# Kernel optimization log

Measured on AMD Instinct MI355X. Metric: run time of the kernel, lower is better.

The kernel has to match this reference:

```python
import jax, jax.numpy as jnp
import numpy as np

B, S, D_IN, D_OUT, ENC, K = 4, 2048, 4096, 4096, 256, 2048


def setup_inputs() -> dict:
    key = jax.random.key(0)
    ks = jax.random.split(key, 10)
    return {
        "x": jax.random.normal(ks[0], (B, S, D_IN), jnp.float32),
        "W": jax.random.normal(ks[1], (D_OUT, D_IN), jnp.float32) * 0.02,
        "b": jax.random.normal(ks[2], (D_OUT,), jnp.float32) * 0.02,
        "enc_W1": jax.random.normal(ks[3], (ENC, D_IN), jnp.float32) * 0.02,
        "enc_b1": jax.random.normal(ks[4], (ENC,), jnp.float32) * 0.02,
        "enc_W2": jax.random.normal(ks[5], (ENC, ENC), jnp.float32) * 0.05,
        "enc_b2": jax.random.normal(ks[6], (ENC,), jnp.float32) * 0.02,
        "keys": jax.random.normal(ks[7], (K, ENC), jnp.float32),
        "values": jax.random.normal(ks[8], (K, D_OUT), jnp.float32),
        "epsilons": jax.random.uniform(ks[9], (K,), jnp.float32) * 20.0,
    }


def reference(x, W, b, enc_W1, enc_b1, enc_W2, enc_b2, keys, values, epsilons):
    # 1) wrapped Linear layer: layer_out = x @ W^T + b   [B,S,D_OUT]
    layer_out = jnp.einsum("bsd,od->bso", x, W) + b

    Bv, Sv = x.shape[0], x.shape[1]
    token_to_edit = Sv - 1  # key_id == -1 inference path

    # 2) per-sample first-diff-position detection (vectorized version of the
    #    python loop: first j>=1 with hs[i,j-1] != hs[i,j], 1 remapped to 0,
    #    and 0 when batch size is 1)
    if Bv == 1:
        first = jnp.zeros((Bv,), jnp.int32)
    else:
        diffs = jnp.any(x[:, 1:] != x[:, :-1], axis=-1)  # [B, S-1]
        has = jnp.any(diffs, axis=1)
        first = jnp.where(has, jnp.argmax(diffs, axis=1).astype(jnp.int32) + 1, 0)
        first = jnp.where(first == 1, 0, first)

    # 3) mean over positions [first_diff_pos, token_to_edit] per sample
    pos = jnp.arange(Sv)
    mask = (pos[None, :] >= first[:, None]) & (pos[None, :] <= token_to_edit)
    m = mask[..., None].astype(x.dtype)
    pooled = (x * m).sum(axis=1) / m.sum(axis=1)  # [B, D_IN]

    # 4) encoder MLP: Linear -> ReLU -> Linear  (MLPEncoder(key_shape, 256))
    h = jax.nn.relu(pooled @ enc_W1.T + enc_b1)
    query = h @ enc_W2.T + enc_b2  # [B, ENC]

    # 5) cdist(keys, query, p=2) -> [K, B], nearest key per sample
    d2 = ((keys * keys).sum(1)[:, None]
          + (query * query).sum(1)[None, :]
          - 2.0 * keys @ query.T)
    dists = jnp.sqrt(jnp.maximum(d2, 0.0))  # [K, B]
    smallest_dist = dists.min(axis=0)        # [B]
    chosen_key = dists.argmin(axis=0)        # [B]

    chosen_value = values[chosen_key]        # [B, D_OUT]
    eps = epsilons[chosen_key]               # [B]

    # 6) replacement == 'replace_all'
    hit = (smallest_dist <= eps)[:, None, None]
    out = jnp.where(hit, chosen_value[:, None, :], layer_out)
    return out
```

## Files before the change

### kernel.cpp

```cpp
#include <hip/hip_runtime.h>
#include <cfloat>
#include <climits>


typedef unsigned short u16;
typedef unsigned int   u32;
typedef __attribute__((ext_vector_type(8))) short bf16x8;
typedef __attribute__((ext_vector_type(4))) float f32x4;
typedef __attribute__((address_space(3))) u32 as3u32;
typedef const __attribute__((address_space(1))) u32 as1u32;

#define NB 4
#define NS 2048
#define ND 4096
#define NE 256
#define NK 2048
#define NROWS (NB * NS)

#define OFF_XB     ((size_t)0)
#define OFF_WB     ((size_t)67108864)
#define OFF_FLAGS  ((size_t)100663296)
#define OFF_FIRST  ((size_t)100696064)
#define OFF_INV    ((size_t)100696080)
#define OFF_POOLED ((size_t)100696320)
#define OFF_H      ((size_t)100761856)
#define OFF_Q      ((size_t)100765952)
#define OFF_CD2    ((size_t)100770048)
#define OFF_CIDX   ((size_t)100770560)
#define OFF_HIT    ((size_t)100771072)
#define OFF_CHOSEN ((size_t)100771088)

__device__ __forceinline__ void gld_lds16(const u16* g, u16* l) {
  __builtin_amdgcn_global_load_lds((as1u32*)g, (as3u32*)l, 16, 0, 0);
}

__device__ __forceinline__ u16 f2bf(float f) {
  union { float f; u32 u; } v; v.f = f;
  u32 r = v.u + 0x7fffu + ((v.u >> 16) & 1u);
  return (u16)(r >> 16);
}

__device__ __forceinline__ void mfma_bf16(f32x4& acc, bf16x8 a, bf16x8 b) {
  asm("v_mfma_f32_16x16x32_bf16 %0, %1, %2, %0" : "+v"(acc) : "v"(a), "v"(b));
}

__global__ __launch_bounds__(256) void k_convert(
    const float* __restrict__ x, const float* __restrict__ W,
    u16* __restrict__ xb, u16* __restrict__ wb, int* __restrict__ flags)
{
  int r = blockIdx.x;
  int tid = threadIdx.x;
  bool isX = r < NROWS;
  int s = r & (NS - 1);
  const float* src;
  u16* dst;
  if (isX) { src = x + (size_t)r * ND; dst = xb + (size_t)r * ND; }
  else     { int wr = r - NROWS; src = W + (size_t)wr * ND; dst = wb + (size_t)wr * ND; }

  const float4* s4 = (const float4*)src;
  int b4 = tid * 4;
  float4 v[4];
#pragma unroll
  for (int i = 0; i < 4; i++) v[i] = s4[b4 + i];

  bool d = false;
  if (isX && s > 0) {
    const float4* p4 = s4 - (ND / 4);
#pragma unroll
    for (int i = 0; i < 4; i++) {
      float4 p = p4[b4 + i];
      d = d || (v[i].x != p.x) || (v[i].y != p.y) || (v[i].z != p.z) || (v[i].w != p.w);
    }
  }

  u16 t[16];
#pragma unroll
  for (int i = 0; i < 4; i++) {
    t[i*4+0] = f2bf(v[i].x); t[i*4+1] = f2bf(v[i].y);
    t[i*4+2] = f2bf(v[i].z); t[i*4+3] = f2bf(v[i].w);
  }
  uint4* d4 = (uint4*)(dst + (size_t)tid * 16);
  d4[0] = *(const uint4*)&t[0];
  d4[1] = *(const uint4*)&t[8];

  if (isX) {
    __shared__ int sf;
    if (tid == 0) sf = 0;
    __syncthreads();
    if (__any((int)d) && (tid & 63) == 0) atomicOr(&sf, 1);
    __syncthreads();
    if (tid == 0) flags[r] = (s == 0) ? 0 : sf;
  }
}

__global__ __launch_bounds__(256) void k_first(
    const int* __restrict__ flags, int* __restrict__ first, float* __restrict__ inv)
{
  __shared__ int red[256];
  int tid = threadIdx.x;
  for (int b = 0; b < NB; b++) {
    int best = INT_MAX;
    for (int j = 1 + tid; j < NS; j += 256)
      if (flags[b * NS + j] && j < best) best = j;
    red[tid] = best;
    __syncthreads();
    for (int st = 128; st > 0; st >>= 1) {
      if (tid < st && red[tid + st] < red[tid]) red[tid] = red[tid + st];
      __syncthreads();
    }
    if (tid == 0) {
      int f = red[0];
      if (f == INT_MAX) f = 0;
      if (f == 1) f = 0;
      first[b] = f;
      inv[b] = 1.0f / (float)(NS - f);
    }
    __syncthreads();
  }
}

__global__ __launch_bounds__(256) void k_pool(
    const float* __restrict__ x, const int* __restrict__ first, float* __restrict__ pooled)
{
  int b = blockIdx.x >> 6;
  int tile = blockIdx.x & 63;
  int f = first[b];
  int s0 = tile * 32;
  int tid = threadIdx.x;
  float acc[16];
#pragma unroll
  for (int k = 0; k < 16; k++) acc[k] = 0.f;
  const float* base = x + ((size_t)b * NS + s0) * ND + tid * 16;
  for (int i = 0; i < 32; i++) {
    if (s0 + i >= f) {
      const float4* p = (const float4*)(base + (size_t)i * ND);
#pragma unroll
      for (int j = 0; j < 4; j++) {
        float4 v = p[j];
        acc[j*4+0] += v.x; acc[j*4+1] += v.y; acc[j*4+2] += v.z; acc[j*4+3] += v.w;
      }
    }
  }
  float* dst = pooled + b * ND + tid * 16;
#pragma unroll
  for (int k = 0; k < 16; k++) atomicAdd(&dst[k], acc[k]);
}

__global__ __launch_bounds__(256) void k_enc1(
    const float* __restrict__ pooled, const float* __restrict__ inv,
    const float* __restrict__ W1, const float* __restrict__ b1, float* __restrict__ h)
{
  int o = blockIdx.x, tid = threadIdx.x;
  const float4* w4 = (const float4*)(W1 + (size_t)o * ND);
  float4 w[4];
#pragma unroll
  for (int i = 0; i < 4; i++) w[i] = w4[tid * 4 + i];
  float part[NB];
#pragma unroll
  for (int b = 0; b < NB; b++) {
    const float4* p4 = (const float4*)(pooled + b * ND);
    float s = 0.f;
#pragma unroll
    for (int i = 0; i < 4; i++) {
      float4 p = p4[tid * 4 + i];
      s += w[i].x*p.x + w[i].y*p.y + w[i].z*p.z + w[i].w*p.w;
    }
    part[b] = s;
  }
  __shared__ float red[NB][4];
  int lane = tid & 63, wv = tid >> 6;
#pragma unroll
  for (int b = 0; b < NB; b++) {
    float v = part[b];
    for (int off = 32; off > 0; off >>= 1) v += __shfl_down(v, off);
    if (lane == 0) red[b][wv] = v;
  }
  __syncthreads();
  if (tid < NB) {
    float s = red[tid][0] + red[tid][1] + red[tid][2] + red[tid][3];
    h[tid * NE + o] = fmaxf(s * inv[tid] + b1[o], 0.f);
  }
}

__global__ __launch_bounds__(256) void k_enc2(
    const float* __restrict__ h, const float* __restrict__ W2,
    const float* __restrict__ b2, float* __restrict__ q)
{
  __shared__ float hs[NB * NE];
  int tid = threadIdx.x;
  for (int i = tid; i < NB * NE; i += 256) hs[i] = h[i];
  __syncthreads();
  const float* w = W2 + (size_t)tid * NE;
  float bb = b2[tid];
  float s0 = bb, s1 = bb, s2 = bb, s3 = bb;
  for (int e = 0; e < NE; e++) {
    float wv = w[e];
    s0 += hs[e] * wv; s1 += hs[NE + e] * wv;
    s2 += hs[2*NE + e] * wv; s3 += hs[3*NE + e] * wv;
  }
  q[tid] = s0; q[NE + tid] = s1; q[2*NE + tid] = s2; q[3*NE + tid] = s3;
}

__global__ __launch_bounds__(64) void k_dist(
    const float* __restrict__ keys, const float* __restrict__ q,
    float* __restrict__ cd2, int* __restrict__ cidx)
{
  __shared__ float qs[NB * NE];
  int tid = threadIdx.x;
  for (int i = tid; i < NB * NE; i += 64) qs[i] = q[i];
  __syncthreads();
  int k = blockIdx.x * 64 + tid;
  const float4* kr = (const float4*)(keys + (size_t)k * NE);
  float d2[NB];
#pragma unroll
  for (int b = 0; b < NB; b++) d2[b] = 0.f;
  for (int e4 = 0; e4 < NE / 4; e4++) {
    float4 kv = kr[e4];
#pragma unroll
    for (int b = 0; b < NB; b++) {
      const float4* qv4 = (const float4*)(qs + b * NE);
      float4 qv = qv4[e4];
      float dx = kv.x - qv.x, dy = kv.y - qv.y, dz = kv.z - qv.z, dw = kv.w - qv.w;
      d2[b] += dx*dx + dy*dy + dz*dz + dw*dw;
    }
  }
#pragma unroll
  for (int b = 0; b < NB; b++) {
    float v = d2[b]; int idx = k;
    for (int off = 32; off > 0; off >>= 1) {
      float ov = __shfl_down(v, off);
      int   oi = __shfl_down(idx, off);
      if (ov < v || (ov == v && oi < idx)) { v = ov; idx = oi; }
    }
    if (tid == 0) { cd2[blockIdx.x * NB + b] = v; cidx[blockIdx.x * NB + b] = idx; }
  }
}

__global__ __launch_bounds__(64) void k_decide(
    const float* __restrict__ cd2, const int* __restrict__ cidx,
    const float* __restrict__ eps, int* __restrict__ hit, int* __restrict__ chosen)
{
  int tid = threadIdx.x;
  for (int b = 0; b < NB; b++) {
    float v = FLT_MAX; int idx = INT_MAX;
    if (tid < 32) { v = cd2[tid * NB + b]; idx = cidx[tid * NB + b]; }
    for (int off = 32; off > 0; off >>= 1) {
      float ov = __shfl_down(v, off);
      int   oi = __shfl_down(idx, off);
      if (ov < v || (ov == v && oi < idx)) { v = ov; idx = oi; }
    }
    if (tid == 0) {
      float dist = sqrtf(fmaxf(v, 0.f));
      chosen[b] = idx;
      hit[b] = (dist <= eps[idx]) ? 1 : 0;
    }
  }
}

__global__ __launch_bounds__(256) void k_gemm(
    const u16* __restrict__ A, const u16* __restrict__ Bw,
    const float* __restrict__ bias, const float* __restrict__ values,
    const int* __restrict__ hit, const int* __restrict__ chosen,
    float* __restrict__ out)
{
  __shared__ __align__(16) u16 As[128 * 64];
  __shared__ __align__(16) u16 Bs[128 * 64];
  int tid = threadIdx.x;
  size_t mbase = (size_t)blockIdx.y * 128;
  size_t nbase = (size_t)blockIdx.x * 128;
  int lane = tid & 63, wv = tid >> 6;
  int wm = (wv >> 1) * 64, wn = (wv & 1) * 64;
  int frow = lane & 15, fk = (lane >> 4) * 8;

  f32x4 acc[4][4] = {};

  for (int kt = 0; kt < ND; kt += 64) {
#pragma unroll
    for (int i = 0; i < 4; i++) {
      int c = i * 256 + tid;
      int row = c >> 3, col = (c & 7) * 8;
      gld_lds16(A  + (mbase + row) * ND + kt + col, &As[c * 8]);
      gld_lds16(Bw + (nbase + row) * ND + kt + col, &Bs[c * 8]);
    }
    __syncthreads();
#pragma unroll
    for (int ks = 0; ks < 2; ks++) {
      bf16x8 af[4], bg[4];
      int ko = ks * 32 + fk;
#pragma unroll
      for (int mf = 0; mf < 4; mf++)
        af[mf] = *(const bf16x8*)&As[(wm + mf * 16 + frow) * 64 + ko];
#pragma unroll
      for (int nf = 0; nf < 4; nf++)
        bg[nf] = *(const bf16x8*)&Bs[(wn + nf * 16 + frow) * 64 + ko];
#pragma unroll
      for (int mf = 0; mf < 4; mf++)
#pragma unroll
        for (int nf = 0; nf < 4; nf++)
          mfma_bf16(acc[mf][nf], af[mf], bg[nf]);
    }
    __syncthreads();
  }

  int smp = (int)(mbase >> 11);
  int ht = hit[smp];
  const float* vrow = values + (size_t)chosen[smp] * ND;
  int r0 = (lane >> 4) * 4, c0 = lane & 15;
#pragma unroll
  for (int mf = 0; mf < 4; mf++) {
    size_t m = mbase + wm + mf * 16 + r0;
#pragma unroll
    for (int nf = 0; nf < 4; nf++) {
      size_t o = nbase + wn + nf * 16 + c0;
      float bia = bias[o];
      float rep = ht ? vrow[o] : 0.f;
#pragma unroll
      for (int r = 0; r < 4; r++) {
        float vvv = acc[mf][nf][r] + bia;
        out[(m + r) * ND + o] = ht ? rep : vvv;
      }
    }
  }
}

extern "C" void kernel_launch(void* const* d_in, const int* in_sizes, int n_in,
                              void* d_out, int out_size, void* d_ws, size_t ws_size,
                              hipStream_t stream) {
  const float* x      = (const float*)d_in[0];
  const float* W      = (const float*)d_in[1];
  const float* bias   = (const float*)d_in[2];
  const float* W1     = (const float*)d_in[3];
  const float* b1     = (const float*)d_in[4];
  const float* W2     = (const float*)d_in[5];
  const float* b2     = (const float*)d_in[6];
  const float* keys   = (const float*)d_in[7];
  const float* values = (const float*)d_in[8];
  const float* eps    = (const float*)d_in[9];
  float* out = (float*)d_out;
  char* ws = (char*)d_ws;

  u16*   xb     = (u16*)(ws + OFF_XB);
  u16*   wb     = (u16*)(ws + OFF_WB);
  int*   flags  = (int*)(ws + OFF_FLAGS);
  int*   first  = (int*)(ws + OFF_FIRST);
  float* inv    = (float*)(ws + OFF_INV);
  float* pooled = (float*)(ws + OFF_POOLED);
  float* h      = (float*)(ws + OFF_H);
  float* q      = (float*)(ws + OFF_Q);
  float* cd2    = (float*)(ws + OFF_CD2);
  int*   cidx   = (int*)(ws + OFF_CIDX);
  int*   hitp   = (int*)(ws + OFF_HIT);
  int*   chosenp= (int*)(ws + OFF_CHOSEN);

  hipMemsetAsync(pooled, 0, NB * ND * sizeof(float), stream);

  k_convert<<<NROWS + ND, 256, 0, stream>>>(x, W, xb, wb, flags);
  k_first  <<<1, 256, 0, stream>>>(flags, first, inv);
  k_pool   <<<256, 256, 0, stream>>>(x, first, pooled);
  k_enc1   <<<NE, 256, 0, stream>>>(pooled, inv, W1, b1, h);
  k_enc2   <<<1, 256, 0, stream>>>(h, W2, b2, q);
  k_dist   <<<NK / 64, 64, 0, stream>>>(keys, q, cd2, cidx);
  k_decide <<<1, 64, 0, stream>>>(cd2, cidx, eps, hitp, chosenp);

  dim3 gg(ND / 128, NROWS / 128);
  k_gemm<<<gg, 256, 0, stream>>>(xb, wb, bias, values, hitp, chosenp, out);
}
```

Before: 741.9 us.

## Rewrite pipeline: fuse pooling into prep, 256x256 ping-pong GEMM, atomic argmin

```diff
diff --git a/kernel.cpp b/kernel.cpp
--- a/kernel.cpp
+++ b/kernel.cpp
@@ -5,6 +5,7 @@
 
 typedef unsigned short u16;
 typedef unsigned int   u32;
+typedef unsigned long long u64;
 typedef __attribute__((ext_vector_type(8))) short bf16x8;
 typedef __attribute__((ext_vector_type(4))) float f32x4;
 typedef __attribute__((address_space(3))) u32 as3u32;
@@ -16,19 +17,17 @@
 #define NE 256
 #define NK 2048
 #define NROWS (NB * NS)
+#define NT 64
 
 #define OFF_XB     ((size_t)0)
 #define OFF_WB     ((size_t)67108864)
-#define OFF_FLAGS  ((size_t)100663296)
-#define OFF_FIRST  ((size_t)100696064)
-#define OFF_INV    ((size_t)100696080)
-#define OFF_POOLED ((size_t)100696320)
-#define OFF_H      ((size_t)100761856)
-#define OFF_Q      ((size_t)100765952)
-#define OFF_CD2    ((size_t)100770048)
-#define OFF_CIDX   ((size_t)100770560)
-#define OFF_HIT    ((size_t)100771072)
-#define OFF_CHOSEN ((size_t)100771088)
+#define OFF_TS     ((size_t)100663296)
+#define OFF_FLAGS  ((size_t)104857600)
+#define OFF_FIRST  ((size_t)104890368)
+#define OFF_INV    ((size_t)104890384)
+#define OFF_MINPK  ((size_t)104890400)
+#define OFF_POOLED ((size_t)104890432)
+#define OFF_H      ((size_t)104955968)
 
 __device__ __forceinline__ void gld_lds16(const u16* g, u16* l) {
   __builtin_amdgcn_global_load_lds((as1u32*)g, (as3u32*)l, 16, 0, 0);
@@ -44,60 +43,86 @@
   asm("v_mfma_f32_16x16x32_bf16 %0, %1, %2, %0" : "+v"(acc) : "v"(a), "v"(b));
 }
 
-__global__ __launch_bounds__(256) void k_convert(
+__global__ __launch_bounds__(256) void k_prep(
     const float* __restrict__ x, const float* __restrict__ W,
-    u16* __restrict__ xb, u16* __restrict__ wb, int* __restrict__ flags)
-{
-  int r = blockIdx.x;
-  int tid = threadIdx.x;
-  bool isX = r < NROWS;
-  int s = r & (NS - 1);
-  const float* src;
-  u16* dst;
-  if (isX) { src = x + (size_t)r * ND; dst = xb + (size_t)r * ND; }
-  else     { int wr = r - NROWS; src = W + (size_t)wr * ND; dst = wb + (size_t)wr * ND; }
-
-  const float4* s4 = (const float4*)src;
-  int b4 = tid * 4;
-  float4 v[4];
-#pragma unroll
-  for (int i = 0; i < 4; i++) v[i] = s4[b4 + i];
-
-  bool d = false;
-  if (isX && s > 0) {
-    const float4* p4 = s4 - (ND / 4);
-#pragma unroll
-    for (int i = 0; i < 4; i++) {
-      float4 p = p4[b4 + i];
-      d = d || (v[i].x != p.x) || (v[i].y != p.y) || (v[i].z != p.z) || (v[i].w != p.w);
-    }
-  }
-
-  u16 t[16];
-#pragma unroll
-  for (int i = 0; i < 4; i++) {
-    t[i*4+0] = f2bf(v[i].x); t[i*4+1] = f2bf(v[i].y);
-    t[i*4+2] = f2bf(v[i].z); t[i*4+3] = f2bf(v[i].w);
-  }
-  uint4* d4 = (uint4*)(dst + (size_t)tid * 16);
-  d4[0] = *(const uint4*)&t[0];
-  d4[1] = *(const uint4*)&t[8];
-
-  if (isX) {
-    __shared__ int sf;
-    if (tid == 0) sf = 0;
-    __syncthreads();
-    if (__any((int)d) && (tid & 63) == 0) atomicOr(&sf, 1);
-    __syncthreads();
-    if (tid == 0) flags[r] = (s == 0) ? 0 : sf;
-  }
+    u16* __restrict__ xb, u16* __restrict__ wb,
+    int* __restrict__ flags, float* __restrict__ ts)
+{
+  int blk = blockIdx.x, tid = threadIdx.x;
+  if (blk >= 256) {
+    int wr0 = (blk - 256) * 16;
+    for (int i = 0; i < 16; i++) {
+      const float* rp = W + (size_t)(wr0 + i) * ND;
+      u16* op = wb + (size_t)(wr0 + i) * ND;
+#pragma unroll
+      for (int ch = 0; ch < 4; ch++) {
+        int col = ch * 1024 + tid * 4;
+        float4 v = *(const float4*)(rp + col);
+        uint2 pk;
+        pk.x = (u32)f2bf(v.x) | ((u32)f2bf(v.y) << 16);
+        pk.y = (u32)f2bf(v.z) | ((u32)f2bf(v.w) << 16);
+        *(uint2*)(op + col) = pk;
+      }
+    }
+    return;
+  }
+  int b = blk >> 6, tile = blk & 63, s0 = tile * 32;
+  __shared__ int rflag[32];
+  if (tid < 32) rflag[tid] = 0;
+  __syncthreads();
+  float prev[16];
+  bool havePrev = (s0 > 0);
+  if (havePrev) {
+    const float* pr = x + ((size_t)b * NS + s0 - 1) * ND;
+#pragma unroll
+    for (int ch = 0; ch < 4; ch++)
+      *(float4*)&prev[ch * 4] = *(const float4*)(pr + ch * 1024 + tid * 4);
+  }
+  float tsa[16];
+#pragma unroll
+  for (int k = 0; k < 16; k++) tsa[k] = 0.f;
+  for (int i = 0; i < 32; i++) {
+    size_t row = (size_t)b * NS + s0 + i;
+    const float* rp = x + row * ND;
+    u16* op = xb + row * ND;
+    float cur[16];
+#pragma unroll
+    for (int ch = 0; ch < 4; ch++) {
+      int col = ch * 1024 + tid * 4;
+      float4 v = *(const float4*)(rp + col);
+      cur[ch*4+0] = v.x; cur[ch*4+1] = v.y; cur[ch*4+2] = v.z; cur[ch*4+3] = v.w;
+      uint2 pk;
+      pk.x = (u32)f2bf(v.x) | ((u32)f2bf(v.y) << 16);
+      pk.y = (u32)f2bf(v.z) | ((u32)f2bf(v.w) << 16);
+      *(uint2*)(op + col) = pk;
+    }
+    if (havePrev || i > 0) {
+      bool d = false;
+#pragma unroll
+      for (int k = 0; k < 16; k++) d = d || (cur[k] != prev[k]);
+      if (__any((int)d) && (tid & 63) == 0) atomicOr(&rflag[i], 1);
+    }
+#pragma unroll
+    for (int k = 0; k < 16; k++) { tsa[k] += cur[k]; prev[k] = cur[k]; }
+  }
+  float* tsp = ts + (size_t)(b * 64 + tile) * ND;
+#pragma unroll
+  for (int ch = 0; ch < 4; ch++) {
+    int col = ch * 1024 + tid * 4;
+    float4 v; v.x = tsa[ch*4+0]; v.y = tsa[ch*4+1]; v.z = tsa[ch*4+2]; v.w = tsa[ch*4+3];
+    *(float4*)(tsp + col) = v;
+  }
+  __syncthreads();
+  if (tid < 32) flags[b * NS + s0 + tid] = rflag[tid];
 }
 
 __global__ __launch_bounds__(256) void k_first(
-    const int* __restrict__ flags, int* __restrict__ first, float* __restrict__ inv)
+    const int* __restrict__ flags, int* __restrict__ first, float* __restrict__ inv,
+    u64* __restrict__ minpk)
 {
   __shared__ int red[256];
   int tid = threadIdx.x;
+  if (tid < NB) minpk[tid] = 0xFFFFFFFFFFFFFFFFull;
   for (int b = 0; b < NB; b++) {
     int best = INT_MAX;
     for (int j = 1 + tid; j < NS; j += 256)
@@ -119,35 +144,30 @@
   }
 }
 
-__global__ __launch_bounds__(256) void k_pool(
-    const float* __restrict__ x, const int* __restrict__ first, float* __restrict__ pooled)
-{
-  int b = blockIdx.x >> 6;
-  int tile = blockIdx.x & 63;
-  int f = first[b];
-  int s0 = tile * 32;
-  int tid = threadIdx.x;
-  float acc[16];
-#pragma unroll
-  for (int k = 0; k < 16; k++) acc[k] = 0.f;
-  const float* base = x + ((size_t)b * NS + s0) * ND + tid * 16;
-  for (int i = 0; i < 32; i++) {
-    if (s0 + i >= f) {
-      const float4* p = (const float4*)(base + (size_t)i * ND);
-#pragma unroll
-      for (int j = 0; j < 4; j++) {
-        float4 v = p[j];
-        acc[j*4+0] += v.x; acc[j*4+1] += v.y; acc[j*4+2] += v.z; acc[j*4+3] += v.w;
-      }
-    }
-  }
-  float* dst = pooled + b * ND + tid * 16;
-#pragma unroll
-  for (int k = 0; k < 16; k++) atomicAdd(&dst[k], acc[k]);
+__global__ __launch_bounds__(256) void k_poolfix(
+    const float* __restrict__ x, const float* __restrict__ ts,
+    const int* __restrict__ first, const float* __restrict__ inv,
+    float* __restrict__ pooled)
+{
+  int b = blockIdx.x >> 2, seg = blockIdx.x & 3;
+  int col = seg * 1024 + threadIdx.x * 4;
+  int f = first[b], tf = f >> 5;
+  float4 s = {0.f, 0.f, 0.f, 0.f};
+  for (int t = tf; t < 64; t++) {
+    float4 v = *(const float4*)(ts + (size_t)(b * 64 + t) * ND + col);
+    s.x += v.x; s.y += v.y; s.z += v.z; s.w += v.w;
+  }
+  for (int r = tf * 32; r < f; r++) {
+    float4 v = *(const float4*)(x + ((size_t)b * NS + r) * ND + col);
+    s.x -= v.x; s.y -= v.y; s.z -= v.z; s.w -= v.w;
+  }
+  float iv = inv[b];
+  float4 o; o.x = s.x * iv; o.y = s.y * iv; o.z = s.z * iv; o.w = s.w * iv;
+  *(float4*)(pooled + (size_t)b * ND + col) = o;
 }
 
 __global__ __launch_bounds__(256) void k_enc1(
-    const float* __restrict__ pooled, const float* __restrict__ inv,
+    const float* __restrict__ pooled,
     const float* __restrict__ W1, const float* __restrict__ b1, float* __restrict__ h)
 {
   int o = blockIdx.x, tid = threadIdx.x;
@@ -158,7 +178,7 @@
   float part[NB];
 #pragma unroll
   for (int b = 0; b < NB; b++) {
-    const float4* p4 = (const float4*)(pooled + b * ND);
+    const float4* p4 = (const float4*)(pooled + (size_t)b * ND);
     float s = 0.f;
 #pragma unroll
     for (int i = 0; i < 4; i++) {
@@ -168,146 +188,197 @@
     part[b] = s;
   }
   __shared__ float red[NB][4];
-  int lane = tid & 63, wv = tid >> 6;
+  int lane = tid & 63, wvv = tid >> 6;
 #pragma unroll
   for (int b = 0; b < NB; b++) {
     float v = part[b];
     for (int off = 32; off > 0; off >>= 1) v += __shfl_down(v, off);
-    if (lane == 0) red[b][wv] = v;
+    if (lane == 0) red[b][wvv] = v;
   }
   __syncthreads();
   if (tid < NB) {
     float s = red[tid][0] + red[tid][1] + red[tid][2] + red[tid][3];
-    h[tid * NE + o] = fmaxf(s * inv[tid] + b1[o], 0.f);
-  }
-}
-
-__global__ __launch_bounds__(256) void k_enc2(
+    h[tid * NE + o] = fmaxf(s + b1[o], 0.f);
+  }
+}
+
+__global__ __launch_bounds__(256) void k_dist2(
     const float* __restrict__ h, const float* __restrict__ W2,
-    const float* __restrict__ b2, float* __restrict__ q)
+    const float* __restrict__ b2, const float* __restrict__ keys,
+    u64* __restrict__ minpk)
 {
   __shared__ float hs[NB * NE];
+  __shared__ float qs[NB][NE];
   int tid = threadIdx.x;
   for (int i = tid; i < NB * NE; i += 256) hs[i] = h[i];
   __syncthreads();
-  const float* w = W2 + (size_t)tid * NE;
-  float bb = b2[tid];
-  float s0 = bb, s1 = bb, s2 = bb, s3 = bb;
-  for (int e = 0; e < NE; e++) {
-    float wv = w[e];
-    s0 += hs[e] * wv; s1 += hs[NE + e] * wv;
-    s2 += hs[2*NE + e] * wv; s3 += hs[3*NE + e] * wv;
-  }
-  q[tid] = s0; q[NE + tid] = s1; q[2*NE + tid] = s2; q[3*NE + tid] = s3;
-}
-
-__global__ __launch_bounds__(64) void k_dist(
-    const float* __restrict__ keys, const float* __restrict__ q,
-    float* __restrict__ cd2, int* __restrict__ cidx)
-{
-  __shared__ float qs[NB * NE];
-  int tid = threadIdx.x;
-  for (int i = tid; i < NB * NE; i += 64) qs[i] = q[i];
+  {
+    const float4* w4 = (const float4*)(W2 + (size_t)tid * NE);
+    float bb = b2[tid];
+    float s0 = bb, s1 = bb, s2 = bb, s3 = bb;
+    for (int e4 = 0; e4 < NE / 4; e4++) {
+      float4 wv = w4[e4];
+      float4 a0 = ((const float4*)(hs))[e4];
+      float4 a1 = ((const float4*)(hs + NE))[e4];
+      float4 a2 = ((const float4*)(hs + 2 * NE))[e4];
+      float4 a3 = ((const float4*)(hs + 3 * NE))[e4];
+      s0 += wv.x*a0.x + wv.y*a0.y + wv.z*a0.z + wv.w*a0.w;
+      s1 += wv.x*a1.x + wv.y*a1.y + wv.z*a1.z + wv.w*a1.w;
+      s2 += wv.x*a2.x + wv.y*a2.y + wv.z*a2.z + wv.w*a2.w;
+      s3 += wv.x*a3.x + wv.y*a3.y + wv.z*a3.z + wv.w*a3.w;
+    }
+    qs[0][tid] = s0; qs[1][tid] = s1; qs[2][tid] = s2; qs[3][tid] = s3;
+  }
   __syncthreads();
-  int k = blockIdx.x * 64 + tid;
-  const float4* kr = (const float4*)(keys + (size_t)k * NE);
-  float d2[NB];
-#pragma unroll
-  for (int b = 0; b < NB; b++) d2[b] = 0.f;
-  for (int e4 = 0; e4 < NE / 4; e4++) {
-    float4 kv = kr[e4];
+  if (tid < 64) {
+    int k = blockIdx.x * 64 + tid;
+    const float4* kr = (const float4*)(keys + (size_t)k * NE);
+    float d2[NB] = {0.f, 0.f, 0.f, 0.f};
+    for (int e4 = 0; e4 < NE / 4; e4++) {
+      float4 kv = kr[e4];
+#pragma unroll
+      for (int b = 0; b < NB; b++) {
+        float4 qv = ((const float4*)&qs[b][0])[e4];
+        float dx = kv.x - qv.x, dy = kv.y - qv.y, dz = kv.z - qv.z, dw = kv.w - qv.w;
+        d2[b] += dx*dx + dy*dy + dz*dz + dw*dw;
+      }
+    }
 #pragma unroll
     for (int b = 0; b < NB; b++) {
-      const float4* qv4 = (const float4*)(qs + b * NE);
-      float4 qv = qv4[e4];
-      float dx = kv.x - qv.x, dy = kv.y - qv.y, dz = kv.z - qv.z, dw = kv.w - qv.w;
-      d2[b] += dx*dx + dy*dy + dz*dz + dw*dw;
-    }
-  }
-#pragma unroll
-  for (int b = 0; b < NB; b++) {
-    float v = d2[b]; int idx = k;
-    for (int off = 32; off > 0; off >>= 1) {
-      float ov = __shfl_down(v, off);
-      int   oi = __shfl_down(idx, off);
-      if (ov < v || (ov == v && oi < idx)) { v = ov; idx = oi; }
-    }
-    if (tid == 0) { cd2[blockIdx.x * NB + b] = v; cidx[blockIdx.x * NB + b] = idx; }
-  }
-}
-
-__global__ __launch_bounds__(64) void k_decide(
-    const float* __restrict__ cd2, const int* __restrict__ cidx,
-    const float* __restrict__ eps, int* __restrict__ hit, int* __restrict__ chosen)
-{
-  int tid = threadIdx.x;
-  for (int b = 0; b < NB; b++) {
-    float v = FLT_MAX; int idx = INT_MAX;
-    if (tid < 32) { v = cd2[tid * NB + b]; idx = cidx[tid * NB + b]; }
-    for (int off = 32; off > 0; off >>= 1) {
-      float ov = __shfl_down(v, off);
-      int   oi = __shfl_down(idx, off);
-      if (ov < v || (ov == v && oi < idx)) { v = ov; idx = oi; }
-    }
-    if (tid == 0) {
-      float dist = sqrtf(fmaxf(v, 0.f));
-      chosen[b] = idx;
-      hit[b] = (dist <= eps[idx]) ? 1 : 0;
-    }
-  }
-}
-
-__global__ __launch_bounds__(256) void k_gemm(
+      float v = d2[b]; int idx = k;
+      for (int off = 32; off > 0; off >>= 1) {
+        float ov = __shfl_down(v, off);
+        int   oi = __shfl_down(idx, off);
+        if (ov < v || (ov == v && oi < idx)) { v = ov; idx = oi; }
+      }
+      if (tid == 0)
+        atomicMin(&minpk[b], ((u64)__float_as_uint(v) << 32) | (u32)idx);
+    }
+  }
+}
+
+__device__ __forceinline__ void stage_half(const u16* __restrict__ mat, size_t rowbase,
+                                           u16* slot, int ktile, int kh, int tid) {
+  int wv = tid >> 6, lane = tid & 63;
+#pragma unroll
+  for (int r = 0; r < 2; r++) {
+    int ci = wv + 8 * r;
+    int lrow = ci * 16 + (lane >> 2);
+    int kc = (lane & 3) ^ ((lrow >> 1) & 3);
+    const u16* src = mat + (rowbase + lrow) * ND + (ktile * 64 + kh * 32 + kc * 8);
+    gld_lds16(src, slot + ci * 512 + lane * 8);
+  }
+}
+
+__device__ __forceinline__ bf16x8 ld_frag(const u16* slot, int row, int kc) {
+  int chunk = kc ^ ((row >> 1) & 3);
+  return *(const bf16x8*)(slot + row * 32 + chunk * 8);
+}
+
+__global__ __launch_bounds__(512, 2) void k_gemm(
     const u16* __restrict__ A, const u16* __restrict__ Bw,
     const float* __restrict__ bias, const float* __restrict__ values,
-    const int* __restrict__ hit, const int* __restrict__ chosen,
+    const u64* __restrict__ minpk, const float* __restrict__ eps,
     float* __restrict__ out)
 {
-  __shared__ __align__(16) u16 As[128 * 64];
-  __shared__ __align__(16) u16 Bs[128 * 64];
-  int tid = threadIdx.x;
-  size_t mbase = (size_t)blockIdx.y * 128;
-  size_t nbase = (size_t)blockIdx.x * 128;
-  int lane = tid & 63, wv = tid >> 6;
-  int wm = (wv >> 1) * 64, wn = (wv & 1) * 64;
-  int frow = lane & 15, fk = (lane >> 4) * 8;
-
-  f32x4 acc[4][4] = {};
-
-  for (int kt = 0; kt < ND; kt += 64) {
-#pragma unroll
-    for (int i = 0; i < 4; i++) {
-      int c = i * 256 + tid;
-      int row = c >> 3, col = (c & 7) * 8;
-      gld_lds16(A  + (mbase + row) * ND + kt + col, &As[c * 8]);
-      gld_lds16(Bw + (nbase + row) * ND + kt + col, &Bs[c * 8]);
-    }
-    __syncthreads();
-#pragma unroll
-    for (int ks = 0; ks < 2; ks++) {
-      bf16x8 af[4], bg[4];
-      int ko = ks * 32 + fk;
-#pragma unroll
-      for (int mf = 0; mf < 4; mf++)
-        af[mf] = *(const bf16x8*)&As[(wm + mf * 16 + frow) * 64 + ko];
-#pragma unroll
-      for (int nf = 0; nf < 4; nf++)
-        bg[nf] = *(const bf16x8*)&Bs[(wn + nf * 16 + frow) * 64 + ko];
-#pragma unroll
-      for (int mf = 0; mf < 4; mf++)
-#pragma unroll
-        for (int nf = 0; nf < 4; nf++)
-          mfma_bf16(acc[mf][nf], af[mf], bg[nf]);
-    }
-    __syncthreads();
-  }
-
-  int smp = (int)(mbase >> 11);
-  int ht = hit[smp];
-  const float* vrow = values + (size_t)chosen[smp] * ND;
+  __shared__ __align__(16) u16 As[2][2][256 * 32];
+  __shared__ __align__(16) u16 Bs[2][2][256 * 32];
+  int tid = threadIdx.x, lane = tid & 63, wv = tid >> 6;
+  size_t mbase = (size_t)blockIdx.y * 256;
+  size_t nbase = (size_t)blockIdx.x * 256;
+  int wm = (wv >> 2) * 128, wn = (wv & 3) * 64;
+  int frow = lane & 15, fkc = lane >> 4;
+
+  f32x4 acc[8][4] = {};
+
+  stage_half(Bw, nbase, Bs[0][0], 0, 0, tid);
+  stage_half(A,  mbase, As[0][0], 0, 0, tid);
+  stage_half(Bw, nbase, Bs[0][1], 0, 1, tid);
+  stage_half(A,  mbase, As[0][1], 0, 1, tid);
+  stage_half(Bw, nbase, Bs[1][0], 1, 0, tid);
+  stage_half(A,  mbase, As[1][0], 1, 0, tid);
+  stage_half(Bw, nbase, Bs[1][1], 1, 1, tid);
+  asm volatile("s_waitcnt vmcnt(6)" ::: "memory");
+  __builtin_amdgcn_s_barrier();
+
+  bf16x8 afr[4], bfr[4];
+  for (int t = 0; t < NT; t++) {
+    int c = t & 1;
+    int kt1 = (t + 1 < NT) ? t + 1 : NT - 1;
+    int kt2 = (t + 2 < NT) ? t + 2 : NT - 1;
+    const u16* Ac0 = As[c][0]; const u16* Ac1 = As[c][1];
+    const u16* Bc0 = Bs[c][0]; const u16* Bc1 = Bs[c][1];
+
+#pragma unroll
+    for (int mf = 0; mf < 4; mf++) afr[mf] = ld_frag(Ac0, wm + mf * 16 + frow, fkc);
+#pragma unroll
+    for (int nf = 0; nf < 4; nf++) bfr[nf] = ld_frag(Bc0, wn + nf * 16 + frow, fkc);
+    stage_half(A, mbase, As[c ^ 1][1], kt1, 1, tid);
+    __builtin_amdgcn_s_barrier();
+    asm volatile("s_waitcnt lgkmcnt(0)" ::: "memory");
+    __builtin_amdgcn_sched_barrier(0);
+    __builtin_amdgcn_s_setprio(1);
+#pragma unroll
+    for (int mf = 0; mf < 4; mf++)
+#pragma unroll
+      for (int nf = 0; nf < 4; nf++) mfma_bf16(acc[mf][nf], afr[mf], bfr[nf]);
+    __builtin_amdgcn_s_setprio(0);
+    __builtin_amdgcn_s_barrier();
+
+#pragma unroll
+    for (int mf = 0; mf < 4; mf++) afr[mf] = ld_frag(Ac0, wm + 64 + mf * 16 + frow, fkc);
+    stage_half(Bw, nbase, Bs[c][0], kt2, 0, tid);
+    __builtin_amdgcn_s_barrier();
+    asm volatile("s_waitcnt lgkmcnt(0)" ::: "memory");
+    __builtin_amdgcn_sched_barrier(0);
+    __builtin_amdgcn_s_setprio(1);
+#pragma unroll
+    for (int mf = 0; mf < 4; mf++)
+#pragma unroll
+      for (int nf = 0; nf < 4; nf++) mfma_bf16(acc[4 + mf][nf], afr[mf], bfr[nf]);
+    __builtin_amdgcn_s_setprio(0);
+    __builtin_amdgcn_s_barrier();
+
+#pragma unroll
+    for (int mf = 0; mf < 4; mf++) afr[mf] = ld_frag(Ac1, wm + mf * 16 + frow, fkc);
+#pragma unroll
+    for (int nf = 0; nf < 4; nf++) bfr[nf] = ld_frag(Bc1, wn + nf * 16 + frow, fkc);
+    stage_half(A, mbase, As[c][0], kt2, 0, tid);
+    __builtin_amdgcn_s_barrier();
+    asm volatile("s_waitcnt lgkmcnt(0)" ::: "memory");
+    __builtin_amdgcn_sched_barrier(0);
+    __builtin_amdgcn_s_setprio(1);
+#pragma unroll
+    for (int mf = 0; mf < 4; mf++)
+#pragma unroll
+      for (int nf = 0; nf < 4; nf++) mfma_bf16(acc[mf][nf], afr[mf], bfr[nf]);
+    __builtin_amdgcn_s_setprio(0);
+    __builtin_amdgcn_s_barrier();
+
+#pragma unroll
+    for (int mf = 0; mf < 4; mf++) afr[mf] = ld_frag(Ac1, wm + 64 + mf * 16 + frow, fkc);
+    stage_half(Bw, nbase, Bs[c][1], kt2, 1, tid);
+    __builtin_amdgcn_s_barrier();
+    asm volatile("s_waitcnt lgkmcnt(0)" ::: "memory");
+    __builtin_amdgcn_sched_barrier(0);
+    __builtin_amdgcn_s_setprio(1);
+#pragma unroll
+    for (int mf = 0; mf < 4; mf++)
+#pragma unroll
+      for (int nf = 0; nf < 4; nf++) mfma_bf16(acc[4 + mf][nf], afr[mf], bfr[nf]);
+    __builtin_amdgcn_s_setprio(0);
+    asm volatile("s_waitcnt vmcnt(6)" ::: "memory");
+    __builtin_amdgcn_s_barrier();
+  }
+
+  u64 pk = minpk[mbase >> 11];
+  float d2 = __uint_as_float((u32)(pk >> 32));
+  int idx = (int)(pk & 0xFFFFFFFFull);
+  int ht = (sqrtf(fmaxf(d2, 0.f)) <= eps[idx]) ? 1 : 0;
+  const float* vrow = values + (size_t)idx * ND;
   int r0 = (lane >> 4) * 4, c0 = lane & 15;
 #pragma unroll
-  for (int mf = 0; mf < 4; mf++) {
+  for (int mf = 0; mf < 8; mf++) {
     size_t m = mbase + wm + mf * 16 + r0;
 #pragma unroll
     for (int nf = 0; nf < 4; nf++) {
@@ -315,10 +386,8 @@
       float bia = bias[o];
       float rep = ht ? vrow[o] : 0.f;
 #pragma unroll
-      for (int r = 0; r < 4; r++) {
-        float vvv = acc[mf][nf][r] + bia;
-        out[(m + r) * ND + o] = ht ? rep : vvv;
-      }
+      for (int r = 0; r < 4; r++)
+        out[(m + r) * ND + o] = ht ? rep : (acc[mf][nf][r] + bia);
     }
   }
 }
@@ -341,27 +410,20 @@
 
   u16*   xb     = (u16*)(ws + OFF_XB);
   u16*   wb     = (u16*)(ws + OFF_WB);
+  float* ts     = (float*)(ws + OFF_TS);
   int*   flags  = (int*)(ws + OFF_FLAGS);
   int*   first  = (int*)(ws + OFF_FIRST);
   float* inv    = (float*)(ws + OFF_INV);
+  u64*   minpk  = (u64*)(ws + OFF_MINPK);
   float* pooled = (float*)(ws + OFF_POOLED);
   float* h      = (float*)(ws + OFF_H);
-  float* q      = (float*)(ws + OFF_Q);
-  float* cd2    = (float*)(ws + OFF_CD2);
-  int*   cidx   = (int*)(ws + OFF_CIDX);
-  int*   hitp   = (int*)(ws + OFF_HIT);
-  int*   chosenp= (int*)(ws + OFF_CHOSEN);
-
-  hipMemsetAsync(pooled, 0, NB * ND * sizeof(float), stream);
-
-  k_convert<<<NROWS + ND, 256, 0, stream>>>(x, W, xb, wb, flags);
-  k_first  <<<1, 256, 0, stream>>>(flags, first, inv);
-  k_pool   <<<256, 256, 0, stream>>>(x, first, pooled);
-  k_enc1   <<<NE, 256, 0, stream>>>(pooled, inv, W1, b1, h);
-  k_enc2   <<<1, 256, 0, stream>>>(h, W2, b2, q);
-  k_dist   <<<NK / 64, 64, 0, stream>>>(keys, q, cd2, cidx);
-  k_decide <<<1, 64, 0, stream>>>(cd2, cidx, eps, hitp, chosenp);
-
-  dim3 gg(ND / 128, NROWS / 128);
-  k_gemm<<<gg, 256, 0, stream>>>(xb, wb, bias, values, hitp, chosenp, out);
-}
+
+  k_prep   <<<512, 256, 0, stream>>>(x, W, xb, wb, flags, ts);
+  k_first  <<<1, 256, 0, stream>>>(flags, first, inv, minpk);
+  k_poolfix<<<16, 256, 0, stream>>>(x, ts, first, inv, pooled);
+  k_enc1   <<<NE, 256, 0, stream>>>(pooled, W1, b1, h);
+  k_dist2  <<<NK / 64, 256, 0, stream>>>(h, W2, b2, keys, minpk);
+
+  dim3 gg(ND / 256, NROWS / 256);
+  k_gemm<<<gg, 512, 0, stream>>>(xb, wb, bias, values, minpk, eps, out);
+}
```

Result: faster. 707.6 us (-4.6%).
